# Optimization experiments

Measured on AMD Instinct MI355X. Metric: run time of the kernel, lower is better.

Reference implementation:

```python
import jax, jax.numpy as jnp
import numpy as np

FEATURE_W = 1.0
TRIPLET_W = 1.0
MARGIN = 0.5
CE_W = 1.0
CE_TEMP = 0.1
DIR_W = 1.0
EPS_VALID = 1e-6
EPS_NORM = 1e-8


def setup_inputs() -> dict:
    key = jax.random.key(0)
    k1, k2, k3, k4, k5 = jax.random.split(key, 5)
    B, C, T, K = 8, 512, 1500, 4096
    return {
        "student_out": jax.random.normal(k1, (B, C, T), dtype=jnp.float32),
        "teacher_out": jax.random.normal(k2, (B, C, T), dtype=jnp.float32),
        "codebook": jax.random.normal(k3, (K, C), dtype=jnp.float32),
        "teacher_codes": jax.random.randint(k4, (B, T), 0, K, dtype=jnp.int64),
        "original_encoder_out": jax.random.normal(k5, (B, C, T), dtype=jnp.float32),
    }


def reference(student_out, teacher_out, codebook, teacher_codes, original_encoder_out):
    B, C, T = student_out.shape
    K = codebook.shape[0]
    N = B * T

    # ---- feature MSE ----
    feature_loss = jnp.mean((student_out - teacher_out) ** 2)

    # ---- triplet with hard negative mining ----
    z = jnp.transpose(student_out, (0, 2, 1)).reshape(N, C)  # (N, C)
    tgt = teacher_codes.reshape(N)
    # squared L2 distances (argmin-equivalent to cdist since sqrt is monotone)
    z2 = jnp.sum(z * z, axis=1, keepdims=True)            # (N, 1)
    c2 = jnp.sum(codebook * codebook, axis=1)             # (K,)
    d2 = z2 - 2.0 * (z @ codebook.T) + c2[None, :]        # (N, K)
    d2 = d2.at[jnp.arange(N), tgt].set(jnp.inf)           # exclude correct code
    hard_idx = jnp.argmin(d2, axis=1)                     # (N,)
    hard_negatives = codebook[hard_idx].reshape(B, T, C)

    anchor = jnp.transpose(teacher_out, (0, 2, 1))        # (B, T, C)
    positive = jnp.transpose(student_out, (0, 2, 1))
    d_pos = jnp.linalg.norm(anchor - positive, axis=-1)   # (B, T)
    d_neg = jnp.linalg.norm(anchor - hard_negatives, axis=-1)
    triplet_loss = jnp.mean(jax.nn.relu(d_pos - d_neg + MARGIN))

    # ---- CE over codebook (negative squared distance logits) ----
    logits = (2.0 * (z @ codebook.T) - c2[None, :]) / CE_TEMP  # (N, K)
    logp = jax.nn.log_softmax(logits, axis=-1)
    ce_loss = -jnp.mean(jnp.take_along_axis(logp, tgt[:, None], axis=1))

    # ---- direction-aware loss ----
    movement = jnp.transpose(student_out - original_encoder_out, (0, 2, 1)).reshape(N, C)
    direction = jnp.transpose(teacher_out - original_encoder_out, (0, 2, 1)).reshape(N, C)
    m_norm = jnp.linalg.norm(movement, axis=-1, keepdims=True)
    d_norm = jnp.linalg.norm(direction, axis=-1, keepdims=True)
    valid = (m_norm[:, 0] > EPS_VALID) & (d_norm[:, 0] > EPS_VALID)  # (N,)
    cos = jnp.sum((movement / (m_norm + EPS_NORM)) * (direction / (d_norm + EPS_NORM)), axis=-1)
    n_valid = jnp.sum(valid)
    dir_cos_loss = jnp.sum(jnp.where(valid, 1.0 - cos, 0.0)) / jnp.maximum(n_valid, 1).astype(cos.dtype)
    dir_mse = jnp.mean((student_out - teacher_out) ** 2)
    direction_loss = dir_mse + 1.0 * dir_cos_loss  # DirectionAwareLoss(direction_weight=1.0)

    total = (FEATURE_W * feature_loss + TRIPLET_W * triplet_loss
             + CE_W * ce_loss + DIR_W * direction_loss)
    return total
```

## Files before the change

kernel.cpp:

```cpp
#include <hip/hip_runtime.h>
#include <math.h>

#define NN 12000
#define NP 12032
#define CCD 512
#define KK 4096
#define TT 1500
#define S20F 28.853900817779268f
#define SC2F 14.426950408889634f
#define LN2F 0.6931471805599453f

typedef float f32x4 __attribute__((ext_vector_type(4)));
typedef __bf16 bf16x8 __attribute__((ext_vector_type(8)));

#if __has_builtin(__builtin_amdgcn_exp2f)
#define EXP2(x) __builtin_amdgcn_exp2f(x)
#else
static __device__ __forceinline__ float exp2_asm(float x){
  float r; asm("v_exp_f32 %0, %1" : "=v"(r) : "v"(x)); return r;
}
#define EXP2(x) exp2_asm(x)
#endif

__device__ __forceinline__ ushort f2bf(float f){
  uint u = __float_as_uint(f);
  uint r = (u + 0x7fffu + ((u >> 16) & 1u)) >> 16;
  return (ushort)r;
}

typedef __attribute__((address_space(1))) const unsigned int g_u32;
typedef __attribute__((address_space(3))) unsigned int l_u32;
__device__ __forceinline__ void gload_lds16(const void* g, void* l){
  __builtin_amdgcn_global_load_lds((g_u32*)g, (l_u32*)l, 16, 0, 0);
}

__global__ __launch_bounds__(256) void k_prep_z(const float* __restrict__ src, ushort* __restrict__ dst){
  __shared__ float tile[64][65];
  int b = blockIdx.z, c0 = blockIdx.y*64, t0 = blockIdx.x*64;
  const float* sb = src + ((size_t)b*CCD + c0)*TT + t0;
  for (int i = 0; i < 16; ++i){
    int e = i*256 + threadIdx.x;
    int cl = e >> 6, tl = e & 63;
    if (t0 + tl < TT) tile[cl][tl] = sb[(size_t)cl*TT + tl];
  }
  __syncthreads();
  for (int i = 0; i < 16; ++i){
    int e = i*256 + threadIdx.x;
    int tl = e >> 6, cl = e & 63;
    if (t0 + tl < TT) dst[((size_t)b*TT + t0 + tl)*CCD + c0 + cl] = f2bf(tile[cl][tl]);
  }
}

__global__ __launch_bounds__(256) void k_prep_cb(const float* __restrict__ cb,
    ushort* __restrict__ cbsw, float* __restrict__ c2s){
  int id = blockIdx.x*256 + threadIdx.x;
  int l     = id & 63;
  int kstep = (id >> 6) & 15;
  int tile  = id >> 10;
  int code  = tile*16 + (l & 15);
  int cc    = kstep*32 + (l >> 4)*8;
  const float* src = cb + ((size_t)code*CCD + cc);
  float4 v0 = *(const float4*)src;
  float4 v1 = *(const float4*)(src + 4);
  uint4 o;
  o.x = (uint)f2bf(v0.x) | ((uint)f2bf(v0.y) << 16);
  o.y = (uint)f2bf(v0.z) | ((uint)f2bf(v0.w) << 16);
  o.z = (uint)f2bf(v1.x) | ((uint)f2bf(v1.y) << 16);
  o.w = (uint)f2bf(v1.z) | ((uint)f2bf(v1.w) << 16);
  ((uint4*)cbsw)[id] = o;
  float s = v0.x*v0.x + v0.y*v0.y + v0.z*v0.z + v0.w*v0.w
          + v1.x*v1.x + v1.y*v1.y + v1.z*v1.z + v1.w*v1.w;
  s += __shfl_xor(s, 16);
  s += __shfl_xor(s, 32);
  if ((l >> 4) == 0) atomicAdd(&c2s[code], s * SC2F);
}

__global__ __launch_bounds__(256) void k_dist(const ushort* __restrict__ zbf,
    const ushort* __restrict__ cbsw, const float* __restrict__ c2s,
    const int* __restrict__ codes, float4* __restrict__ pstate){
  __shared__ char cs[2*16384];
  int tid = threadIdx.x, w = tid >> 6, l = tid & 63;
  int lm = l & 15, k16 = l >> 4;
  int yk = blockIdx.x, xb = blockIdx.y;
  int n0 = xb * 128, kb = yk * 512;

  bf16x8 A0[16], A1[16];
  {
    const ushort* a0 = zbf + (size_t)(n0 + w*32 + lm)*CCD + k16*8;
#pragma unroll
    for (int u = 0; u < 16; ++u){
      A0[u] = *(const bf16x8*)(a0 + u*32);
      A1[u] = *(const bf16x8*)(a0 + 16*CCD + u*32);
    }
  }
  int tgt[8];
#pragma unroll
  for (int fi=0; fi<2; ++fi)
#pragma unroll
    for (int r=0; r<4; ++r){
      int n = n0 + w*32 + fi*16 + k16*4 + r;
      tgt[fi*4+r] = (n < NN) ? codes[n] : -1;
    }

  float m2[8], ss[8], bv[8]; int bi[8];
#pragma unroll
  for (int i=0;i<8;++i){ m2[i]=-3.0e38f; ss[i]=0.f; bv[i]=-3.0e38f; bi[i]=0x7fffffff; }

#define STAGE(tile, buf) { \
    const char* tb_ = (const char*)cbsw + ((size_t)(yk*32 + (tile)))*16384; \
    _Pragma("unroll") \
    for (int j_ = 0; j_ < 4; ++j_) \
      gload_lds16(tb_ + j_*4096 + tid*16, (buf) + j_*4096 + tid*16); }

  STAGE(0, cs)
  __syncthreads();

#pragma unroll 2
  for (int t = 0; t < 32; ++t){
    const char* cur = cs + (t & 1)*16384;
    char* nxt = cs + ((t + 1) & 1)*16384;
    if (t < 31) STAGE(t + 1, nxt)

    f32x4 a0e = (f32x4){0.f,0.f,0.f,0.f}, a0o = a0e, a1e = a0e, a1o = a0e;
    const char* pb = cur + l*16;
    __builtin_amdgcn_s_setprio(1);
#pragma unroll
    for (int ks = 0; ks < 16; ks += 2){
      bf16x8 b0 = *(const bf16x8*)(pb + ks*1024);
      bf16x8 b1 = *(const bf16x8*)(pb + ks*1024 + 1024);
      a0e = __builtin_amdgcn_mfma_f32_16x16x32_bf16(A0[ks],   b0, a0e, 0,0,0);
      a1e = __builtin_amdgcn_mfma_f32_16x16x32_bf16(A1[ks],   b0, a1e, 0,0,0);
      a0o = __builtin_amdgcn_mfma_f32_16x16x32_bf16(A0[ks+1], b1, a0o, 0,0,0);
      a1o = __builtin_amdgcn_mfma_f32_16x16x32_bf16(A1[ks+1], b1, a1o, 0,0,0);
    }
    __builtin_amdgcn_s_setprio(0);

    int c0g = kb + t*16 + lm;
    float c2r0 = c2s[c0g];
    f32x4 accf[2];
    accf[0] = a0e + a0o;
    accf[1] = a1e + a1o;
#pragma unroll
    for (int fi=0; fi<2; ++fi)
#pragma unroll
    for (int r=0; r<4; ++r){
      int i8 = fi*4 + r;
      float v0 = fmaf(accf[fi][r], S20F, -c2r0);
      if (c0g != tgt[i8] && v0 > bv[i8]){ bv[i8] = v0; bi[i8] = c0g; }
      float d = v0 - m2[i8];
      float e = EXP2(-fabsf(d));
      ss[i8] = (d > 0.f) ? fmaf(ss[i8], e, 1.f) : (ss[i8] + e);
      m2[i8] = fmaxf(m2[i8], v0);
    }
    __syncthreads();
  }
#undef STAGE

#pragma unroll
  for (int off = 1; off < 16; off <<= 1){
#pragma unroll
    for (int i=0; i<8; ++i){
      float mo = __shfl_xor(m2[i], off);
      float so = __shfl_xor(ss[i], off);
      float bvo = __shfl_xor(bv[i], off);
      int  bio = __shfl_xor(bi[i], off);
      if (bvo > bv[i] || (bvo == bv[i] && bio < bi[i])){ bv[i] = bvo; bi[i] = bio; }
      float mn = fmaxf(m2[i], mo);
      ss[i] = ss[i]*EXP2(m2[i]-mn) + so*EXP2(mo-mn);
      m2[i] = mn;
    }
  }
  if (lm == 0){
#pragma unroll
    for (int fi=0; fi<2; ++fi)
#pragma unroll
    for (int r=0; r<4; ++r){
      int i8 = fi*4 + r;
      int row = w*32 + fi*16 + k16*4 + r;
      pstate[(size_t)yk*NP + n0 + row] =
          make_float4(m2[i8], ss[i8], bv[i8], __int_as_float(bi[i8]));
    }
  }
}

__global__ __launch_bounds__(256) void k_final(const float* __restrict__ student,
    const float* __restrict__ teacher, const float* __restrict__ orig,
    const float* __restrict__ cb, const float4* __restrict__ pstate,
    const int* __restrict__ codes, const float* __restrict__ c2s,
    float* __restrict__ accs){
  __shared__ float red[6][4][64];
  __shared__ int   sh_hard[64];
  __shared__ float sh_lse[64];
  int tt = threadIdx.x & 63, cg = threadIdx.x >> 6;
  int n = blockIdx.x*64 + tt;
  bool ok = (n < NN);
  if (cg == 0){
    float m=-3.0e38f, s=0.f, bvv=-3.0e38f; int bii=0x7fffffff;
    if (ok){
      for (int sp = 0; sp < 8; ++sp){
        float4 p = pstate[(size_t)sp*NP + n];
        int pb = __float_as_int(p.w);
        if (p.z > bvv || (p.z == bvv && pb < bii)){ bvv = p.z; bii = pb; }
        float mn = fmaxf(m, p.x);
        s = s*EXP2(m - mn) + p.y*EXP2(p.x - mn);
        m = mn;
      }
    } else { bii = 0; s = 1.f; m = 0.f; }
    sh_hard[tt] = bii;
    sh_lse[tt]  = m + log2f(s);
  }
  __syncthreads();
  float dp2=0,dn2=0,mm=0,dd=0,md=0,dt=0;
  int tg = 0;
  if (ok){
    int hn = sh_hard[tt]; tg = codes[n];
    int b = n / TT, t = n - b*TT;
    size_t base = (size_t)b*CCD*TT + t;
    const float* ch = cb + (size_t)hn*CCD;
    const float* ct = cb + (size_t)tg*CCD;
    for (int c = cg*128; c < cg*128+128; ++c){
      float sv = student[base + (size_t)c*TT];
      float tv = teacher[base + (size_t)c*TT];
      float ov = orig[base + (size_t)c*TT];
      float cv = ch[c], wv = ct[c];
      float u = sv - tv; dp2 = fmaf(u,u,dp2);
      float v = tv - cv; dn2 = fmaf(v,v,dn2);
      float mv = sv - ov, dv = tv - ov;
      mm = fmaf(mv,mv,mm); dd = fmaf(dv,dv,dd); md = fmaf(mv,dv,md);
      dt = fmaf(sv, wv, dt);
    }
  }
  red[0][cg][tt]=dp2; red[1][cg][tt]=dn2; red[2][cg][tt]=mm;
  red[3][cg][tt]=dd;  red[4][cg][tt]=md;  red[5][cg][tt]=dt;
  __syncthreads();
  if (cg == 0){
    dp2 = red[0][0][tt]+red[0][1][tt]+red[0][2][tt]+red[0][3][tt];
    dn2 = red[1][0][tt]+red[1][1][tt]+red[1][2][tt]+red[1][3][tt];
    mm  = red[2][0][tt]+red[2][1][tt]+red[2][2][tt]+red[2][3][tt];
    dd  = red[3][0][tt]+red[3][1][tt]+red[3][2][tt]+red[3][3][tt];
    md  = red[4][0][tt]+red[4][1][tt]+red[4][2][tt]+red[4][3][tt];
    dt  = red[5][0][tt]+red[5][1][tt]+red[5][2][tt]+red[5][3][tt];
    float trip=0.f, dc=0.f, nv=0.f, ce=0.f;
    if (ok){
      float dpos = sqrtf(dp2), dneg = sqrtf(dn2);
      trip = fmaxf(dpos - dneg + 0.5f, 0.f);
      float mn = sqrtf(mm), dnn = sqrtf(dd);
      bool valid = (mn > 1e-6f) && (dnn > 1e-6f);
      float cosv = md / ((mn + 1e-8f)*(dnn + 1e-8f));
      if (valid){ dc = 1.f - cosv; nv = 1.f; }
      ce = sh_lse[tt] - (fmaf(dt, S20F, -c2s[tg]));
    }
    for (int off=1; off<64; off<<=1){
      trip += __shfl_xor(trip,off);
      dc   += __shfl_xor(dc,off);
      nv   += __shfl_xor(nv,off);
      dp2  += __shfl_xor(dp2,off);
      ce   += __shfl_xor(ce,off);
    }
    if (tt == 0){
      atomicAdd(&accs[0], trip); atomicAdd(&accs[1], dc);
      atomicAdd(&accs[2], nv);   atomicAdd(&accs[3], dp2);
      atomicAdd(&accs[4], ce);
    }
  }
}

__global__ void k_total(const float* __restrict__ accs, float* __restrict__ out){
  float feat = accs[3] / 6144000.f;
  float trip = accs[0] / (float)NN;
  float ce   = (accs[4] / (float)NN) * LN2F;
  float nv   = accs[2] < 1.f ? 1.f : accs[2];
  float dc   = accs[1] / nv;
  out[0] = 2.f*feat + trip + ce + dc;
}

extern "C" void kernel_launch(void* const* d_in, const int* in_sizes, int n_in,
                              void* d_out, int out_size, void* d_ws, size_t ws_size,
                              hipStream_t stream){
  const float* student = (const float*)d_in[0];
  const float* teacher = (const float*)d_in[1];
  const float* cb      = (const float*)d_in[2];
  const int*   codes   = (const int*)d_in[3];
  const float* orig    = (const float*)d_in[4];

  char* ws = (char*)d_ws;
  ushort* zbf    = (ushort*)(ws);
  ushort* cbsw   = (ushort*)(ws + 12320768);
  float4* pstate = (float4*)(ws + 16515072);
  float*  c2s    = (float*)(ws + 18055168);
  float*  accs   = (float*)(ws + 18071552);
  hipMemsetAsync(ws + 18055168, 0, 16448, stream);
  k_prep_cb<<<1024, 256, 0, stream>>>(cb, cbsw, c2s);
  k_prep_z<<<dim3(24, 8, 8), 256, 0, stream>>>(student, zbf);
  k_dist<<<dim3(8, 94), 256, 0, stream>>>(zbf, cbsw, c2s, codes, pstate);
  k_final<<<188, 256, 0, stream>>>(student, teacher, orig, cb, pstate, codes, c2s, accs);
  k_total<<<1, 1, 0, stream>>>(accs, (float*)d_out);
}
```

Before: 147.2 us.

## Split codebook into 16 slices for k_dist and vectorize k_final over 4 rows

k_dist now covers 256 codes per block instead of 512 and launches 16×94 blocks, so twice as many workgroups share the MFMA work, at the cost of twice as many partial-state records. k_final has each thread handle 4 consecutive time steps using float4 loads of student, teacher and original data, and merges 16 partial states per row. This cuts k_final to 47 blocks, so fewer workgroups each do more work, and the pstate workspace grows, which moves the c2s and accumulator offsets.

Measured after the change: 234.7 us. 59.4% more time.

```diff
diff --git a/kernel.cpp b/kernel.cpp
--- a/kernel.cpp
+++ b/kernel.cpp
@@ -82,7 +82,7 @@
   int tid = threadIdx.x, w = tid >> 6, l = tid & 63;
   int lm = l & 15, k16 = l >> 4;
   int yk = blockIdx.x, xb = blockIdx.y;
-  int n0 = xb * 128, kb = yk * 512;
+  int n0 = xb * 128, kb = yk * 256;
 
   bf16x8 A0[16], A1[16];
   {
@@ -107,7 +107,7 @@
   for (int i=0;i<8;++i){ m2[i]=-3.0e38f; ss[i]=0.f; bv[i]=-3.0e38f; bi[i]=0x7fffffff; }
 
 #define STAGE(tile, buf) { \
-    const char* tb_ = (const char*)cbsw + ((size_t)(yk*32 + (tile)))*16384; \
+    const char* tb_ = (const char*)cbsw + ((size_t)(yk*16 + (tile)))*16384; \
     _Pragma("unroll") \
     for (int j_ = 0; j_ < 4; ++j_) \
       gload_lds16(tb_ + j_*4096 + tid*16, (buf) + j_*4096 + tid*16); }
@@ -116,10 +116,10 @@
   __syncthreads();
 
 #pragma unroll 2
-  for (int t = 0; t < 32; ++t){
+  for (int t = 0; t < 16; ++t){
     const char* cur = cs + (t & 1)*16384;
     char* nxt = cs + ((t + 1) & 1)*16384;
-    if (t < 31) STAGE(t + 1, nxt)
+    if (t < 15) STAGE(t + 1, nxt)
 
     f32x4 a0e = (f32x4){0.f,0.f,0.f,0.f}, a0o = a0e, a1e = a0e, a1o = a0e;
     const char* pb = cur + l*16;
@@ -188,79 +188,94 @@
     const float* __restrict__ cb, const float4* __restrict__ pstate,
     const int* __restrict__ codes, const float* __restrict__ c2s,
     float* __restrict__ accs){
-  __shared__ float red[6][4][64];
-  __shared__ int   sh_hard[64];
-  __shared__ float sh_lse[64];
+  __shared__ f32x4 red[6][4][64];
+  __shared__ int   sh_hard[256];
+  __shared__ float sh_lse[256];
   int tt = threadIdx.x & 63, cg = threadIdx.x >> 6;
-  int n = blockIdx.x*64 + tt;
-  bool ok = (n < NN);
+  int n0 = blockIdx.x*256;
+  int g0 = n0 + 4*tt;
+  bool ok = (g0 < NN);
   if (cg == 0){
-    float m=-3.0e38f, s=0.f, bvv=-3.0e38f; int bii=0x7fffffff;
-    if (ok){
-      for (int sp = 0; sp < 8; ++sp){
-        float4 p = pstate[(size_t)sp*NP + n];
-        int pb = __float_as_int(p.w);
-        if (p.z > bvv || (p.z == bvv && pb < bii)){ bvv = p.z; bii = pb; }
-        float mn = fmaxf(m, p.x);
-        s = s*EXP2(m - mn) + p.y*EXP2(p.x - mn);
-        m = mn;
+#pragma unroll
+    for (int j = 0; j < 4; ++j){
+      int n = g0 + j;
+      float m=-3.0e38f, s=0.f, bvv=-3.0e38f; int bii=0x7fffffff;
+      if (ok){
+        for (int sp = 0; sp < 16; ++sp){
+          float4 p = pstate[(size_t)sp*NP + n];
+          int pb = __float_as_int(p.w);
+          if (p.z > bvv || (p.z == bvv && pb < bii)){ bvv = p.z; bii = pb; }
+          float mn = fmaxf(m, p.x);
+          s = s*EXP2(m - mn) + p.y*EXP2(p.x - mn);
+          m = mn;
+        }
+      } else { bii = 0; s = 1.f; m = 0.f; }
+      sh_hard[4*tt+j] = bii;
+      sh_lse[4*tt+j]  = m + log2f(s);
+    }
+  }
+  __syncthreads();
+  f32x4 dp2 = (f32x4){0.f,0.f,0.f,0.f}, dn2 = dp2, mm = dp2, dd = dp2, md = dp2, dt = dp2;
+  if (ok){
+    int b = g0 / TT, t0 = g0 - b*TT;
+    size_t base = (size_t)b*CCD*TT + t0;
+    const float* ch[4]; const float* ct[4];
+#pragma unroll
+    for (int j = 0; j < 4; ++j){
+      ch[j] = cb + (size_t)sh_hard[4*tt+j]*CCD;
+      ct[j] = cb + (size_t)codes[g0+j]*CCD;
+    }
+    for (int c = cg*128; c < cg*128+128; ++c){
+      f32x4 sv = *(const f32x4*)(student + base + (size_t)c*TT);
+      f32x4 tv = *(const f32x4*)(teacher + base + (size_t)c*TT);
+      f32x4 ov = *(const f32x4*)(orig    + base + (size_t)c*TT);
+#pragma unroll
+      for (int j = 0; j < 4; ++j){
+        float cv = ch[j][c], wv = ct[j][c];
+        float u = sv[j] - tv[j]; dp2[j] = fmaf(u,u,dp2[j]);
+        float v = tv[j] - cv;    dn2[j] = fmaf(v,v,dn2[j]);
+        float mv = sv[j] - ov[j], dv = tv[j] - ov[j];
+        mm[j] = fmaf(mv,mv,mm[j]); dd[j] = fmaf(dv,dv,dd[j]); md[j] = fmaf(mv,dv,md[j]);
+        dt[j] = fmaf(sv[j], wv, dt[j]);
       }
-    } else { bii = 0; s = 1.f; m = 0.f; }
-    sh_hard[tt] = bii;
-    sh_lse[tt]  = m + log2f(s);
-  }
-  __syncthreads();
-  float dp2=0,dn2=0,mm=0,dd=0,md=0,dt=0;
-  int tg = 0;
-  if (ok){
-    int hn = sh_hard[tt]; tg = codes[n];
-    int b = n / TT, t = n - b*TT;
-    size_t base = (size_t)b*CCD*TT + t;
-    const float* ch = cb + (size_t)hn*CCD;
-    const float* ct = cb + (size_t)tg*CCD;
-    for (int c = cg*128; c < cg*128+128; ++c){
-      float sv = student[base + (size_t)c*TT];
-      float tv = teacher[base + (size_t)c*TT];
-      float ov = orig[base + (size_t)c*TT];
-      float cv = ch[c], wv = ct[c];
-      float u = sv - tv; dp2 = fmaf(u,u,dp2);
-      float v = tv - cv; dn2 = fmaf(v,v,dn2);
-      float mv = sv - ov, dv = tv - ov;
-      mm = fmaf(mv,mv,mm); dd = fmaf(dv,dv,dd); md = fmaf(mv,dv,md);
-      dt = fmaf(sv, wv, dt);
     }
   }
   red[0][cg][tt]=dp2; red[1][cg][tt]=dn2; red[2][cg][tt]=mm;
   red[3][cg][tt]=dd;  red[4][cg][tt]=md;  red[5][cg][tt]=dt;
   __syncthreads();
   if (cg == 0){
-    dp2 = red[0][0][tt]+red[0][1][tt]+red[0][2][tt]+red[0][3][tt];
-    dn2 = red[1][0][tt]+red[1][1][tt]+red[1][2][tt]+red[1][3][tt];
-    mm  = red[2][0][tt]+red[2][1][tt]+red[2][2][tt]+red[2][3][tt];
-    dd  = red[3][0][tt]+red[3][1][tt]+red[3][2][tt]+red[3][3][tt];
-    md  = red[4][0][tt]+red[4][1][tt]+red[4][2][tt]+red[4][3][tt];
-    dt  = red[5][0][tt]+red[5][1][tt]+red[5][2][tt]+red[5][3][tt];
-    float trip=0.f, dc=0.f, nv=0.f, ce=0.f;
+    f32x4 DP2 = red[0][0][tt]+red[0][1][tt]+red[0][2][tt]+red[0][3][tt];
+    f32x4 DN2 = red[1][0][tt]+red[1][1][tt]+red[1][2][tt]+red[1][3][tt];
+    f32x4 MM  = red[2][0][tt]+red[2][1][tt]+red[2][2][tt]+red[2][3][tt];
+    f32x4 DD  = red[3][0][tt]+red[3][1][tt]+red[3][2][tt]+red[3][3][tt];
+    f32x4 MD  = red[4][0][tt]+red[4][1][tt]+red[4][2][tt]+red[4][3][tt];
+    f32x4 DT  = red[5][0][tt]+red[5][1][tt]+red[5][2][tt]+red[5][3][tt];
+    float trip=0.f, dcs=0.f, nv=0.f, fsum=0.f, ces=0.f;
     if (ok){
-      float dpos = sqrtf(dp2), dneg = sqrtf(dn2);
-      trip = fmaxf(dpos - dneg + 0.5f, 0.f);
-      float mn = sqrtf(mm), dnn = sqrtf(dd);
-      bool valid = (mn > 1e-6f) && (dnn > 1e-6f);
-      float cosv = md / ((mn + 1e-8f)*(dnn + 1e-8f));
-      if (valid){ dc = 1.f - cosv; nv = 1.f; }
-      ce = sh_lse[tt] - (fmaf(dt, S20F, -c2s[tg]));
+#pragma unroll
+      for (int j = 0; j < 4; ++j){
+        float dpos = sqrtf(DP2[j]), dneg = sqrtf(DN2[j]);
+        trip += fmaxf(dpos - dneg + 0.5f, 0.f);
+        float mn = sqrtf(MM[j]), dnn = sqrtf(DD[j]);
+        bool valid = (mn > 1e-6f) && (dnn > 1e-6f);
+        float cosv = MD[j] / ((mn + 1e-8f)*(dnn + 1e-8f));
+        if (valid){ dcs += 1.f - cosv; nv += 1.f; }
+        fsum += DP2[j];
+        int tg = codes[g0+j];
+        ces += sh_lse[4*tt+j] - (fmaf(DT[j], S20F, -c2s[tg]));
+      }
     }
     for (int off=1; off<64; off<<=1){
       trip += __shfl_xor(trip,off);
-      dc   += __shfl_xor(dc,off);
+      dcs  += __shfl_xor(dcs,off);
       nv   += __shfl_xor(nv,off);
-      dp2  += __shfl_xor(dp2,off);
-      ce   += __shfl_xor(ce,off);
+      fsum += __shfl_xor(fsum,off);
+      ces  += __shfl_xor(ces,off);
     }
     if (tt == 0){
-      atomicAdd(&accs[0], trip); atomicAdd(&accs[1], dc);
-      atomicAdd(&accs[2], nv);   atomicAdd(&accs[3], dp2);
-      atomicAdd(&accs[4], ce);
+      atomicAdd(&accs[0], trip); atomicAdd(&accs[1], dcs);
+      atomicAdd(&accs[2], nv);   atomicAdd(&accs[3], fsum);
+      atomicAdd(&accs[4], ces);
     }
   }
 }
@@ -287,12 +302,12 @@
   ushort* zbf    = (ushort*)(ws);
   ushort* cbsw   = (ushort*)(ws + 12320768);
   float4* pstate = (float4*)(ws + 16515072);
-  float*  c2s    = (float*)(ws + 18055168);
-  float*  accs   = (float*)(ws + 18071552);
-  hipMemsetAsync(ws + 18055168, 0, 16448, stream);
+  float*  c2s    = (float*)(ws + 19595264);
+  float*  accs   = (float*)(ws + 19611648);
+  hipMemsetAsync(ws + 19595264, 0, 16448, stream);
   k_prep_cb<<<1024, 256, 0, stream>>>(cb, cbsw, c2s);
   k_prep_z<<<dim3(24, 8, 8), 256, 0, stream>>>(student, zbf);
-  k_dist<<<dim3(8, 94), 256, 0, stream>>>(zbf, cbsw, c2s, codes, pstate);
-  k_final<<<188, 256, 0, stream>>>(student, teacher, orig, cb, pstate, codes, c2s, accs);
+  k_dist<<<dim3(16, 94), 256, 0, stream>>>(zbf, cbsw, c2s, codes, pstate);
+  k_final<<<47, 256, 0, stream>>>(student, teacher, orig, cb, pstate, codes, c2s, accs);
   k_total<<<1, 1, 0, stream>>>(accs, (float*)d_out);
 }
```
